# Kernel optimization log

Measured on AMD Instinct MI355X. Metric: run time of the kernel, lower is better.

Reference implementation:

```python
import jax, jax.numpy as jnp
import numpy as np

LOG2 = float(np.log(2.0))

def ssp(x):
    # schnetpack shifted softplus
    return jax.nn.softplus(x) - LOG2

def gather_neighbors(x, neighbors):
    # x: [B, A, F], neighbors: [B, A, N] int -> [B, A, N, F]
    B, A, N = neighbors.shape
    flat = neighbors.reshape(B, A * N)
    g = jnp.take_along_axis(x, flat[..., None], axis=1)
    return g.reshape(B, A, N, x.shape[-1])

def setup_inputs() -> dict:
    key = jax.random.key(0)
    ks = jax.random.split(key, 6)
    B, A, N, n_in, h = 32, 512, 256, 256, 128
    positions = jax.random.normal(ks[0], (B, A, 3), dtype=jnp.float32) * 3.0
    representation = jax.random.normal(ks[1], (B, A, n_in), dtype=jnp.float32)
    # neighbors guaranteed != self index to avoid zero distances
    off = jax.random.randint(ks[2], (B, A, N), 1, A)
    neighbors = (jnp.arange(A, dtype=jnp.int64)[None, :, None] + off.astype(jnp.int64)) % A
    nbh_mask = jnp.ones((B, A, N), dtype=jnp.float32)
    atom_mask = jnp.ones((B, A), dtype=jnp.float32)
    W1 = jax.random.normal(ks[3], (n_in, h), dtype=jnp.float32) / np.sqrt(n_in)
    b1 = jnp.zeros((h,), dtype=jnp.float32)
    W2 = jax.random.normal(ks[4], (h, 2), dtype=jnp.float32) / np.sqrt(h)
    b2 = jnp.zeros((2,), dtype=jnp.float32)
    return {"positions": positions, "representation": representation,
            "neighbors": neighbors, "nbh_mask": nbh_mask, "atom_mask": atom_mask,
            "W1": W1, "b1": b1, "W2": W2, "b2": b2}

def reference(positions, representation, neighbors, nbh_mask, atom_mask, W1, b1, W2, b2):
    # atom-wise MLP contributions: [B, A, 2]
    contrib = ssp(representation @ W1 + b1) @ W2 + b2

    # pairwise vectors/distances (neighbor - center): [B, A, N, 3], [B, A, N]
    pos_j = gather_neighbors(positions, neighbors)
    dist_vecs = pos_j - positions[:, :, None, :]
    distances = jnp.sqrt(jnp.sum(dist_vecs * dist_vecs, axis=-1))

    # gather neighbor contributions: [B, A, N, 2]
    nc = gather_neighbors(contrib, neighbors)
    nc1 = nc[..., 0]
    nc2 = nc[..., 1]

    # atomic dipoles: masked neighbor sum of dist_vecs * nc1 -> [B, A, 3]
    m = nbh_mask[..., None]
    atomic_dipoles = jnp.sum(dist_vecs * nc1[..., None] * m, axis=2)

    # distance-weighted fields
    masked_dist = distances ** 3 * nbh_mask + (1.0 - nbh_mask)
    nbh_fields = dist_vecs * nc2[..., None] / masked_dist[..., None]
    atomic_fields = jnp.sum(nbh_fields * m, axis=2)  # [B, A, 3]

    # normalize fields (guard tiny norms)
    field_norm = jnp.linalg.norm(atomic_fields, axis=-1, keepdims=True)
    field_norm = field_norm + (field_norm < 1e-10).astype(atomic_fields.dtype)
    atomic_fields = atomic_fields / field_norm

    # symmetric outer product: [B, A, 3, 3]
    ap = atomic_dipoles[..., None] * atomic_fields[:, :, None, :]
    atomic_polar = 0.5 * (ap + jnp.swapaxes(ap, -1, -2))

    # masked sum over atoms -> [B, 3, 3]
    global_polar = jnp.sum(atomic_polar * atom_mask[:, :, None, None], axis=1)
    return global_polar
```

## Files before the change

kernel.cpp:

```cpp
#include <hip/hip_runtime.h>
#include <math.h>

#define BATCH 32
#define NATOM 512
#define NNBH  256
#define NIN   256
#define NH    128

typedef __attribute__((ext_vector_type(8))) short bf16x8;
typedef __attribute__((ext_vector_type(4))) float f32x4;

__device__ __forceinline__ short f2bf(float f) {
    union { float f; unsigned u; } v; v.f = f;
    unsigned r = v.u + 0x7FFFu + ((v.u >> 16) & 1u);
    return (short)(r >> 16);
}

__global__ __launch_bounds__(256) void pack_w1(const float* __restrict__ W1,
                                               short* __restrict__ W1p) {
    int t = blockIdx.x * 256 + threadIdx.x;
    int h    = t & 7;
    int lane = (t >> 3) & 63;
    int n    = (t >> 9) & 7;
    int kb   = t >> 12;
    int k = kb * 32 + (lane >> 4) * 8 + h;
    int j = n * 16 + (lane & 15);
    W1p[t] = f2bf(W1[k * NH + j]);
}

__global__ __launch_bounds__(512, 4) void mlp_mfma(
    const float* __restrict__ rep,
    const short* __restrict__ W1p,
    const float* __restrict__ b1,
    const float* __restrict__ W2,
    const float* __restrict__ b2,
    float* __restrict__ contrib)
{
    __shared__ short sA[32][264];
    __shared__ float part[4][32][2];

    const int tid    = threadIdx.x;
    const int lane   = tid & 63;
    const int wave   = tid >> 6;
    const int rstrip = wave & 1;
    const int npair  = wave >> 1;
    const int rowBase = blockIdx.x * 32;
    const int r0 = lane & 15;
    const int kg = lane >> 4;

    {
        const int r  = tid >> 4;
        const int c0 = (tid & 15) * 16;
        const float4* src = (const float4*)(rep + (size_t)(rowBase + r) * NIN + c0);
        const float4 v0 = src[0], v1 = src[1], v2 = src[2], v3 = src[3];
        bf16x8 h0, h1;
        h0[0] = f2bf(v0.x); h0[1] = f2bf(v0.y); h0[2] = f2bf(v0.z); h0[3] = f2bf(v0.w);
        h0[4] = f2bf(v1.x); h0[5] = f2bf(v1.y); h0[6] = f2bf(v1.z); h0[7] = f2bf(v1.w);
        h1[0] = f2bf(v2.x); h1[1] = f2bf(v2.y); h1[2] = f2bf(v2.z); h1[3] = f2bf(v2.w);
        h1[4] = f2bf(v3.x); h1[5] = f2bf(v3.y); h1[6] = f2bf(v3.z); h1[7] = f2bf(v3.w);
        *(bf16x8*)&sA[r][c0]     = h0;
        *(bf16x8*)&sA[r][c0 + 8] = h1;
    }
    __syncthreads();

    f32x4 acc[2];
    acc[0] = (f32x4){0.f, 0.f, 0.f, 0.f};
    acc[1] = (f32x4){0.f, 0.f, 0.f, 0.f};

    #pragma unroll
    for (int kb = 0; kb < 8; ++kb) {
        const bf16x8 af = *(const bf16x8*)&sA[rstrip * 16 + r0][kb * 32 + kg * 8];
        const bf16x8 bf0 = *(const bf16x8*)(W1p + ((size_t)(kb * 8 + npair * 2 + 0) * 64 + lane) * 8);
        const bf16x8 bf1 = *(const bf16x8*)(W1p + ((size_t)(kb * 8 + npair * 2 + 1) * 64 + lane) * 8);
        acc[0] = __builtin_amdgcn_mfma_f32_16x16x32_bf16(af, bf0, acc[0], 0, 0, 0);
        acc[1] = __builtin_amdgcn_mfma_f32_16x16x32_bf16(af, bf1, acc[1], 0, 0, 0);
    }

    float b1v[2], w20[2], w21[2];
    #pragma unroll
    for (int nn = 0; nn < 2; ++nn) {
        const int j = (npair * 2 + nn) * 16 + r0;
        b1v[nn] = b1[j];
        const float2 w = *(const float2*)(W2 + j * 2);
        w20[nn] = w.x; w21[nn] = w.y;
    }

    float c0[4], c1[4];
    #pragma unroll
    for (int reg = 0; reg < 4; ++reg) {
        float s0 = 0.f, s1 = 0.f;
        #pragma unroll
        for (int nn = 0; nn < 2; ++nn) {
            const float z = acc[nn][reg] + b1v[nn];
            const float hv = fmaxf(z, 0.f) + log1pf(expf(-fabsf(z))) - 0.6931471805599453f;
            s0 = fmaf(hv, w20[nn], s0);
            s1 = fmaf(hv, w21[nn], s1);
        }
        c0[reg] = s0; c1[reg] = s1;
    }

    #pragma unroll
    for (int m = 8; m >= 1; m >>= 1) {
        #pragma unroll
        for (int reg = 0; reg < 4; ++reg) {
            c0[reg] += __shfl_xor(c0[reg], m, 64);
            c1[reg] += __shfl_xor(c1[reg], m, 64);
        }
    }

    if (r0 == 0) {
        #pragma unroll
        for (int reg = 0; reg < 4; ++reg) {
            const int lr = rstrip * 16 + kg * 4 + reg;
            part[npair][lr][0] = c0[reg];
            part[npair][lr][1] = c1[reg];
        }
    }
    __syncthreads();

    if (tid < 64) {
        const int r = tid >> 1;
        const int c = tid & 1;
        const float s = part[0][r][c] + part[1][r][c] + part[2][r][c] + part[3][r][c] + b2[c];
        contrib[(size_t)(rowBase + r) * 2 + c] = s;
    }
}

__global__ __launch_bounds__(256) void pair_kernel(
    const float* __restrict__ positions,
    const int*   __restrict__ neighbors,
    const float* __restrict__ nbh_mask,
    const float* __restrict__ atom_mask,
    const float* __restrict__ contrib,
    float* __restrict__ partials)
{
    const int tid  = threadIdx.x;
    const int wave = tid >> 6;
    const int lane = tid & 63;
    const int atom = blockIdx.x * 4 + wave;
    const int b = atom >> 9;
    const int a = atom & (NATOM - 1);

    const float* posB = positions + (size_t)b * NATOM * 3;
    const float* ctrB = contrib   + (size_t)b * NATOM * 2;
    const float px = posB[a * 3 + 0];
    const float py = posB[a * 3 + 1];
    const float pz = posB[a * 3 + 2];
    const size_t nbase = (size_t)atom * NNBH;

    float dipx = 0.f, dipy = 0.f, dipz = 0.f;
    float fx = 0.f, fy = 0.f, fz = 0.f;

    const int4   idx4 = *(const int4*)(neighbors + nbase + lane * 4);
    const float4 m4   = *(const float4*)(nbh_mask + nbase + lane * 4);
    const int   idxs[4] = {idx4.x, idx4.y, idx4.z, idx4.w};
    const float ms[4]   = {m4.x, m4.y, m4.z, m4.w};

    #pragma unroll
    for (int i = 0; i < 4; ++i) {
        const int idx = idxs[i];
        const float m = ms[i];
        const float qx = posB[idx * 3 + 0];
        const float qy = posB[idx * 3 + 1];
        const float qz = posB[idx * 3 + 2];
        const float2 nc = *(const float2*)(ctrB + idx * 2);
        const float dx = qx - px, dy = qy - py, dz = qz - pz;
        const float d2 = dx * dx + dy * dy + dz * dz;
        const float dist = sqrtf(d2);
        const float md = dist * d2 * m + (1.f - m);
        const float nc1 = nc.x * m;
        const float nc2 = nc.y * m / md;
        dipx = fmaf(dx, nc1, dipx);
        dipy = fmaf(dy, nc1, dipy);
        dipz = fmaf(dz, nc1, dipz);
        fx = fmaf(dx, nc2, fx);
        fy = fmaf(dy, nc2, fy);
        fz = fmaf(dz, nc2, fz);
    }

    #pragma unroll
    for (int off = 32; off >= 1; off >>= 1) {
        dipx += __shfl_down(dipx, off, 64);
        dipy += __shfl_down(dipy, off, 64);
        dipz += __shfl_down(dipz, off, 64);
        fx   += __shfl_down(fx,   off, 64);
        fy   += __shfl_down(fy,   off, 64);
        fz   += __shfl_down(fz,   off, 64);
    }

    __shared__ float sw[4][9];
    if (lane == 0) {
        float norm = sqrtf(fx * fx + fy * fy + fz * fz);
        norm += (norm < 1e-10f) ? 1.f : 0.f;
        const float inv = 1.f / norm;
        const float f0 = fx * inv, f1 = fy * inv, f2 = fz * inv;
        const float am = atom_mask[(size_t)b * NATOM + a];
        const float d0 = dipx, d1 = dipy, d2v = dipz;
        sw[wave][0] = d0 * f0 * am;
        sw[wave][1] = 0.5f * (d0 * f1 + d1 * f0) * am;
        sw[wave][2] = 0.5f * (d0 * f2 + d2v * f0) * am;
        sw[wave][3] = 0.5f * (d1 * f0 + d0 * f1) * am;
        sw[wave][4] = d1 * f1 * am;
        sw[wave][5] = 0.5f * (d1 * f2 + d2v * f1) * am;
        sw[wave][6] = 0.5f * (d2v * f0 + d0 * f2) * am;
        sw[wave][7] = 0.5f * (d2v * f1 + d1 * f2) * am;
        sw[wave][8] = d2v * f2 * am;
    }
    __syncthreads();
    if (tid < 9) {
        partials[(size_t)blockIdx.x * 9 + tid] =
            sw[0][tid] + sw[1][tid] + sw[2][tid] + sw[3][tid];
    }
}

__global__ __launch_bounds__(128) void reduce_kernel(
    const float* __restrict__ partials,
    float* __restrict__ out)
{
    __shared__ float s[128][9];
    const int b = blockIdx.x;
    const int t = threadIdx.x;
    const float* p = partials + (size_t)b * 128 * 9;
    #pragma unroll
    for (int i = 0; i < 9; ++i) s[t][i] = p[(size_t)t * 9 + i];
    __syncthreads();
    if (t < 9) {
        float acc = 0.f;
        #pragma unroll 16
        for (int i = 0; i < 128; ++i) acc += s[i][t];
        out[(size_t)b * 9 + t] = acc;
    }
}

extern "C" void kernel_launch(void* const* d_in, const int* in_sizes, int n_in,
                              void* d_out, int out_size, void* d_ws, size_t ws_size,
                              hipStream_t stream) {
    const float* positions = (const float*)d_in[0];
    const float* rep       = (const float*)d_in[1];
    const int*   neighbors = (const int*)d_in[2];
    const float* nbh_mask  = (const float*)d_in[3];
    const float* atom_mask = (const float*)d_in[4];
    const float* W1        = (const float*)d_in[5];
    const float* b1        = (const float*)d_in[6];
    const float* W2        = (const float*)d_in[7];
    const float* b2        = (const float*)d_in[8];
    float* out = (float*)d_out;

    float* contrib  = (float*)d_ws;
    float* partials = contrib + (size_t)BATCH * NATOM * 2;
    short* W1p      = (short*)(partials + 4096 * 9);

    const int nRows = BATCH * NATOM;

    pack_w1<<<128, 256, 0, stream>>>(W1, W1p);
    mlp_mfma<<<nRows / 32, 512, 0, stream>>>(rep, W1p, b1, W2, b2, contrib);
    pair_kernel<<<nRows / 4, 256, 0, stream>>>(positions, neighbors, nbh_mask, atom_mask,
                                               contrib, partials);
    reduce_kernel<<<BATCH, 128, 0, stream>>>(partials, out);
}
```

Before: 37.67 us.

## Stage per-batch positions and contributions in LDS, process 16 atoms per block

Result: slower. 38.64 us (+2.6%).

```diff
diff --git a/kernel.cpp b/kernel.cpp
--- a/kernel.cpp
+++ b/kernel.cpp
@@ -134,77 +134,104 @@
     const float* __restrict__ contrib,
     float* __restrict__ partials)
 {
-    const int tid  = threadIdx.x;
-    const int wave = tid >> 6;
-    const int lane = tid & 63;
-    const int atom = blockIdx.x * 4 + wave;
-    const int b = atom >> 9;
-    const int a = atom & (NATOM - 1);
+    __shared__ float sp[NATOM * 3];
+    __shared__ float sc[NATOM * 2];
+    __shared__ float sw[4][9];
+
+    const int tid   = threadIdx.x;
+    const int wave  = tid >> 6;
+    const int lane  = tid & 63;
+    const int b     = blockIdx.x >> 5;
+    const int chunk = blockIdx.x & 31;
 
     const float* posB = positions + (size_t)b * NATOM * 3;
     const float* ctrB = contrib   + (size_t)b * NATOM * 2;
-    const float px = posB[a * 3 + 0];
-    const float py = posB[a * 3 + 1];
-    const float pz = posB[a * 3 + 2];
-    const size_t nbase = (size_t)atom * NNBH;
-
-    float dipx = 0.f, dipy = 0.f, dipz = 0.f;
-    float fx = 0.f, fy = 0.f, fz = 0.f;
-
-    const int4   idx4 = *(const int4*)(neighbors + nbase + lane * 4);
-    const float4 m4   = *(const float4*)(nbh_mask + nbase + lane * 4);
-    const int   idxs[4] = {idx4.x, idx4.y, idx4.z, idx4.w};
-    const float ms[4]   = {m4.x, m4.y, m4.z, m4.w};
-
-    #pragma unroll
-    for (int i = 0; i < 4; ++i) {
-        const int idx = idxs[i];
-        const float m = ms[i];
-        const float qx = posB[idx * 3 + 0];
-        const float qy = posB[idx * 3 + 1];
-        const float qz = posB[idx * 3 + 2];
-        const float2 nc = *(const float2*)(ctrB + idx * 2);
-        const float dx = qx - px, dy = qy - py, dz = qz - pz;
-        const float d2 = dx * dx + dy * dy + dz * dz;
-        const float dist = sqrtf(d2);
-        const float md = dist * d2 * m + (1.f - m);
-        const float nc1 = nc.x * m;
-        const float nc2 = nc.y * m / md;
-        dipx = fmaf(dx, nc1, dipx);
-        dipy = fmaf(dy, nc1, dipy);
-        dipz = fmaf(dz, nc1, dipz);
-        fx = fmaf(dx, nc2, fx);
-        fy = fmaf(dy, nc2, fy);
-        fz = fmaf(dz, nc2, fz);
-    }
-
-    #pragma unroll
-    for (int off = 32; off >= 1; off >>= 1) {
-        dipx += __shfl_down(dipx, off, 64);
-        dipy += __shfl_down(dipy, off, 64);
-        dipz += __shfl_down(dipz, off, 64);
-        fx   += __shfl_down(fx,   off, 64);
-        fy   += __shfl_down(fy,   off, 64);
-        fz   += __shfl_down(fz,   off, 64);
-    }
-
-    __shared__ float sw[4][9];
+
+    {
+        const float4* ps = (const float4*)posB;
+        float4* pd = (float4*)sp;
+        pd[tid] = ps[tid];
+        if (tid < 128) pd[256 + tid] = ps[256 + tid];
+        const float4* cs = (const float4*)ctrB;
+        ((float4*)sc)[tid] = cs[tid];
+    }
+    __syncthreads();
+
+    float acc9[9];
+    #pragma unroll
+    for (int i = 0; i < 9; ++i) acc9[i] = 0.f;
+
+    #pragma unroll
+    for (int s = 0; s < 4; ++s) {
+        const int a = chunk * 16 + wave * 4 + s;
+        const float px = sp[a * 3 + 0];
+        const float py = sp[a * 3 + 1];
+        const float pz = sp[a * 3 + 2];
+        const size_t nbase = ((size_t)b * NATOM + a) * NNBH;
+
+        const int4   idx4 = *(const int4*)(neighbors + nbase + lane * 4);
+        const float4 m4   = *(const float4*)(nbh_mask + nbase + lane * 4);
+        const int   idxs[4] = {idx4.x, idx4.y, idx4.z, idx4.w};
+        const float ms[4]   = {m4.x, m4.y, m4.z, m4.w};
+
+        float dipx = 0.f, dipy = 0.f, dipz = 0.f;
+        float fx = 0.f, fy = 0.f, fz = 0.f;
+
+        #pragma unroll
+        for (int i = 0; i < 4; ++i) {
+            const int idx = idxs[i];
+            const float m = ms[i];
+            const float qx = sp[idx * 3 + 0];
+            const float qy = sp[idx * 3 + 1];
+            const float qz = sp[idx * 3 + 2];
+            const float n1 = sc[idx * 2 + 0];
+            const float n2 = sc[idx * 2 + 1];
+            const float dx = qx - px, dy = qy - py, dz = qz - pz;
+            const float d2 = dx * dx + dy * dy + dz * dz;
+            const float dist = sqrtf(d2);
+            const float md = dist * d2 * m + (1.f - m);
+            const float nc1 = n1 * m;
+            const float nc2 = n2 * m / md;
+            dipx = fmaf(dx, nc1, dipx);
+            dipy = fmaf(dy, nc1, dipy);
+            dipz = fmaf(dz, nc1, dipz);
+            fx = fmaf(dx, nc2, fx);
+            fy = fmaf(dy, nc2, fy);
+            fz = fmaf(dz, nc2, fz);
+        }
+
+        #pragma unroll
+        for (int off = 32; off >= 1; off >>= 1) {
+            dipx += __shfl_down(dipx, off, 64);
+            dipy += __shfl_down(dipy, off, 64);
+            dipz += __shfl_down(dipz, off, 64);
+            fx   += __shfl_down(fx,   off, 64);
+            fy   += __shfl_down(fy,   off, 64);
+            fz   += __shfl_down(fz,   off, 64);
+        }
+
+        if (lane == 0) {
+            float norm = sqrtf(fx * fx + fy * fy + fz * fz);
+            norm += (norm < 1e-10f) ? 1.f : 0.f;
+            const float inv = 1.f / norm;
+            const float f0 = fx * inv, f1 = fy * inv, f2 = fz * inv;
+            const float am = atom_mask[(size_t)b * NATOM + a];
+            const float d0 = dipx, d1 = dipy, d2v = dipz;
+            acc9[0] = fmaf(d0 * f0, am, acc9[0]);
+            acc9[1] = fmaf(0.5f * (d0 * f1 + d1 * f0), am, acc9[1]);
+            acc9[2] = fmaf(0.5f * (d0 * f2 + d2v * f0), am, acc9[2]);
+            acc9[3] = fmaf(0.5f * (d1 * f0 + d0 * f1), am, acc9[3]);
+            acc9[4] = fmaf(d1 * f1, am, acc9[4]);
+            acc9[5] = fmaf(0.5f * (d1 * f2 + d2v * f1), am, acc9[5]);
+            acc9[6] = fmaf(0.5f * (d2v * f0 + d0 * f2), am, acc9[6]);
+            acc9[7] = fmaf(0.5f * (d2v * f1 + d1 * f2), am, acc9[7]);
+            acc9[8] = fmaf(d2v * f2, am, acc9[8]);
+        }
+    }
+
     if (lane == 0) {
-        float norm = sqrtf(fx * fx + fy * fy + fz * fz);
-        norm += (norm < 1e-10f) ? 1.f : 0.f;
-        const float inv = 1.f / norm;
-        const float f0 = fx * inv, f1 = fy * inv, f2 = fz * inv;
-        const float am = atom_mask[(size_t)b * NATOM + a];
-        const float d0 = dipx, d1 = dipy, d2v = dipz;
-        sw[wave][0] = d0 * f0 * am;
-        sw[wave][1] = 0.5f * (d0 * f1 + d1 * f0) * am;
-        sw[wave][2] = 0.5f * (d0 * f2 + d2v * f0) * am;
-        sw[wave][3] = 0.5f * (d1 * f0 + d0 * f1) * am;
-        sw[wave][4] = d1 * f1 * am;
-        sw[wave][5] = 0.5f * (d1 * f2 + d2v * f1) * am;
-        sw[wave][6] = 0.5f * (d2v * f0 + d0 * f2) * am;
-        sw[wave][7] = 0.5f * (d2v * f1 + d1 * f2) * am;
-        sw[wave][8] = d2v * f2 * am;
+        #pragma unroll
+        for (int i = 0; i < 9; ++i) sw[wave][i] = acc9[i];
     }
     __syncthreads();
     if (tid < 9) {
@@ -213,21 +240,23 @@
     }
 }
 
-__global__ __launch_bounds__(128) void reduce_kernel(
+__global__ __launch_bounds__(320) void reduce_kernel(
     const float* __restrict__ partials,
     float* __restrict__ out)
 {
-    __shared__ float s[128][9];
+    __shared__ float s[32][9];
     const int b = blockIdx.x;
     const int t = threadIdx.x;
-    const float* p = partials + (size_t)b * 128 * 9;
-    #pragma unroll
-    for (int i = 0; i < 9; ++i) s[t][i] = p[(size_t)t * 9 + i];
+    if (t < 288) {
+        const int i = t / 9;
+        const int j = t - i * 9;
+        s[i][j] = partials[(size_t)(b * 32 + i) * 9 + j];
+    }
     __syncthreads();
     if (t < 9) {
         float acc = 0.f;
-        #pragma unroll 16
-        for (int i = 0; i < 128; ++i) acc += s[i][t];
+        #pragma unroll
+        for (int i = 0; i < 32; ++i) acc += s[i][t];
         out[(size_t)b * 9 + t] = acc;
     }
 }
@@ -248,13 +277,13 @@
 
     float* contrib  = (float*)d_ws;
     float* partials = contrib + (size_t)BATCH * NATOM * 2;
-    short* W1p      = (short*)(partials + 4096 * 9);
+    short* W1p      = (short*)(partials + 1024 * 9);
 
     const int nRows = BATCH * NATOM;
 
     pack_w1<<<128, 256, 0, stream>>>(W1, W1p);
     mlp_mfma<<<nRows / 32, 512, 0, stream>>>(rep, W1p, b1, W2, b2, contrib);
-    pair_kernel<<<nRows / 4, 256, 0, stream>>>(positions, neighbors, nbh_mask, atom_mask,
-                                               contrib, partials);
-    reduce_kernel<<<BATCH, 128, 0, stream>>>(partials, out);
-}
+    pair_kernel<<<BATCH * 32, 256, 0, stream>>>(positions, neighbors, nbh_mask, atom_mask,
+                                                contrib, partials);
+    reduce_kernel<<<BATCH, 320, 0, stream>>>(partials, out);
+}
```
